# Kernel optimization log

Hardware: AMD Instinct MI355X
Metric: run time of the kernel (lower is better)

Reference implementation:

```python
import math
import jax, jax.numpy as jnp
import numpy as np

MUL = 8      # multiplicity of 0e and 1o in irreps_in/out
KS = 5       # kernel spatial extent (diameter 5, steps 1 -> coords -2..2)
NB = 5       # num_radial_basis
RAD = 2.5    # diameter / 2


def _sus(t):
    # e3nn sus(x) = exp(-1/x) for x>0 else 0
    return jnp.where(t > 0.0, jnp.exp(-1.0 / jnp.where(t > 0.0, t, 1.0)), 0.0)


def _emb_sh():
    c = jnp.arange(-2.0, 3.0)
    lat = jnp.stack(jnp.meshgrid(c, c, c, indexing='ij'), axis=-1)  # (5,5,5,3)
    d = jnp.linalg.norm(lat, axis=-1)
    # soft_one_hot_linspace(basis='smooth_finite', cutoff=True)
    values = jnp.linspace(0.0, RAD, NB + 2)
    step = values[1] - values[0]
    diff = (d[..., None] - values[1:-1]) / step
    emb = 1.14136 * math.exp(2.0) * _sus(diff + 1.0) * _sus(1.0 - diff)  # (5,5,5,NB)
    # real spherical harmonics, lmax=2, normalize=True, normalization='component'
    safe = jnp.where(d > 0.0, d, 1.0)[..., None]
    u = jnp.where(d[..., None] > 0.0, lat / safe, 0.0)
    x, y, z = u[..., 0], u[..., 1], u[..., 2]
    s3, s5, s15 = math.sqrt(3.0), math.sqrt(5.0), math.sqrt(15.0)
    sh = jnp.stack([
        jnp.ones_like(x),
        s3 * x, s3 * y, s3 * z,
        s15 * x * z, s15 * x * y,
        s5 * (y * y - 0.5 * (x * x + z * z)),
        s15 * y * z, (s15 / 2.0) * (z * z - x * x),
    ], axis=-1)  # (5,5,5,9)
    return emb, sh


def _c121():
    # Clebsch-Gordan (w3j) for 1o x 2e -> 1o in the real e3nn basis, built from the
    # orthonormal symmetric-traceless matrix basis matching the l=2 SH component order.
    s2, s6 = math.sqrt(2.0), math.sqrt(6.0)
    S = np.zeros((5, 3, 3))
    S[0, 0, 2] = S[0, 2, 0] = 1.0 / s2            # xz
    S[1, 0, 1] = S[1, 1, 0] = 1.0 / s2            # xy
    S[2] = np.diag([-1.0, 2.0, -1.0]) / s6        # 2y^2 - x^2 - z^2
    S[3, 1, 2] = S[3, 2, 1] = 1.0 / s2            # yz
    S[4] = np.diag([-1.0, 0.0, 1.0]) / s2         # z^2 - x^2
    # w3j(1,2,1)[m,j,k] = S[j,m,k]/sqrt(5)  (fully symmetric since l1+l2+l3 even)
    return jnp.asarray(np.transpose(S, (1, 0, 2)) / math.sqrt(5.0), dtype=jnp.float32)


def _build_kernel(weight, emb, sh, c121, dtype):
    g = (KS, KS, KS)
    W = (emb @ weight) / float(KS * KS * KS)  # (5,5,5,320)
    w1, w2, w3, w4, w5 = [W[..., 64 * i:64 * (i + 1)].reshape(g + (MUL, MUL)) for i in range(5)]
    sh0, sh1, sh2 = sh[..., 0], sh[..., 1:4], sh[..., 4:9]
    pw0 = math.sqrt(1.0 / 16.0)   # output 0e: alpha=1, fan_in=8+8
    pw1 = math.sqrt(3.0 / 24.0)   # output 1o: alpha=3, fan_in=8+8+8
    inv_s3 = 1.0 / math.sqrt(3.0)
    K00 = pw0 * sh0[..., None, None] * w1                                   # (g,u,w)
    K01 = (pw1 * inv_s3) * jnp.einsum('xyzuw,xyzk->xyzuwk', w2, sh1)        # (g,u,w,k)
    K10 = (pw0 * inv_s3) * jnp.einsum('xyzuw,xyzm->xyzumw', w4, sh1)        # (g,u,m,w)
    T = jnp.einsum('xyzj,mjk->xyzmk', sh2, c121)                            # (g,m,k)
    eye3 = jnp.eye(3, dtype=dtype)
    K11 = pw1 * (inv_s3 * jnp.einsum('xyzuw,mk->xyzumwk', sh0[..., None, None] * w3, eye3)
                 + jnp.einsum('xyzuw,xyzmk->xyzumwk', w5, T))               # (g,u,m,w,k)
    D = 4 * MUL
    kern = jnp.zeros(g + (D, D), dtype=dtype)
    kern = kern.at[..., :MUL, :MUL].set(K00)
    kern = kern.at[..., :MUL, MUL:].set(K01.reshape(g + (MUL, 3 * MUL)))
    kern = kern.at[..., MUL:, :MUL].set(K10.reshape(g + (3 * MUL, MUL)))
    kern = kern.at[..., MUL:, MUL:].set(K11.reshape(g + (3 * MUL, 3 * MUL)))
    return jnp.transpose(kern, (4, 3, 0, 1, 2))  # 'xyzio->oixyz'


def reference(x, weight, w_sc0, w_sc1):
    emb, sh = _emb_sh()
    c121 = _c121()
    kern = _build_kernel(weight, emb, sh, c121, x.dtype)
    B, _, X, Y, Z = x.shape
    inv_s8 = 1.0 / math.sqrt(MUL)
    # self-connection: e3nn Linear, 0e->0e and 1o->1o blocks
    x0 = x[:, :MUL]
    x1 = x[:, MUL:].reshape(B, MUL, 3, X, Y, Z)
    sc0 = inv_s8 * jnp.einsum('uv,buxyz->bvxyz', w_sc0, x0)
    sc1 = inv_s8 * jnp.einsum('uv,bumxyz->bvmxyz', w_sc1, x1).reshape(B, 3 * MUL, X, Y, Z)
    sc = jnp.concatenate([sc0, sc1], axis=1)
    conv = jax.lax.conv_general_dilated(
        x, kern, window_strides=(1, 1, 1), padding=[(2, 2)] * 3,
        dimension_numbers=('NCDHW', 'OIDHW', 'NCDHW'))
    return sc + conv


def setup_inputs() -> dict:
    key = jax.random.key(0)
    k1, k2, k3, k4 = jax.random.split(key, 4)
    return {
        'x': jax.random.normal(k1, (2, 32, 64, 64, 64), dtype=jnp.float32),
        'weight': jax.random.normal(k2, (NB, 5 * MUL * MUL), dtype=jnp.float32),
        'w_sc0': jax.random.normal(k3, (MUL, MUL), dtype=jnp.float32),
        'w_sc1': jax.random.normal(k4, (MUL, MUL), dtype=jnp.float32),
    }
```

## Files before the change

kernel.cpp:

```cpp
#include <hip/hip_runtime.h>
#include <math.h>

typedef __attribute__((ext_vector_type(8))) short short8;
typedef __attribute__((ext_vector_type(4))) float f32x4;
typedef __attribute__((ext_vector_type(16))) float f32x16;

#define NTAP 125
#define DCH 32

static __device__ __forceinline__ unsigned short f2bf(float f) {
    union { float f; unsigned u; } v; v.f = f;
    unsigned u = v.u;
    return (unsigned short)((u + 0x7FFFu + ((u >> 16) & 1u)) >> 16);
}

static __device__ __forceinline__ void gld_lds16(const void* g, void* l) {
    __builtin_amdgcn_global_load_lds(
        (const __attribute__((address_space(1))) unsigned int*)g,
        (__attribute__((address_space(3))) unsigned int*)l, 16, 0, 0);
}

__global__ __launch_bounds__(128) void build_kern(
    const float* __restrict__ weight,
    const float* __restrict__ w_sc0,
    const float* __restrict__ w_sc1,
    float* __restrict__ kw)
{
    const int t = blockIdx.x;
    const int dx = t / 25, dy = (t / 5) % 5, dz = t % 5;
    const float px = dx - 2.0f, py = dy - 2.0f, pz = dz - 2.0f;
    const float d = sqrtf(px * px + py * py + pz * pz);

    const float stepv = 2.5f / 6.0f;
    const float embc = 1.14136f * expf(2.0f);
    float emb[5];
#pragma unroll
    for (int n = 0; n < 5; ++n) {
        float diff = (d - stepv * (float)(n + 1)) / stepv;
        float a = diff + 1.0f, bb = 1.0f - diff;
        float v = 0.0f;
        if (a > 0.0f && bb > 0.0f)
            v = embc * expf(-1.0f / a) * expf(-1.0f / bb);
        emb[n] = v;
    }

    const float inv_d = (d > 0.0f) ? 1.0f / d : 0.0f;
    const float ux = px * inv_d, uy = py * inv_d, uz = pz * inv_d;
    const float s3 = 1.73205081f, s5 = 2.23606798f, s15 = 3.87298335f;
    float sh[9];
    sh[0] = 1.0f;
    sh[1] = s3 * ux; sh[2] = s3 * uy; sh[3] = s3 * uz;
    sh[4] = s15 * ux * uz;
    sh[5] = s15 * ux * uy;
    sh[6] = s5 * (uy * uy - 0.5f * (ux * ux + uz * uz));
    sh[7] = s15 * uy * uz;
    sh[8] = 0.5f * s15 * (uz * uz - ux * ux);

    const float i_s2 = 0.70710678f, i_s6 = 0.40824829f, i_s5 = 0.44721360f;
    float T[3][3];
    T[0][0] = i_s5 * (-sh[6] * i_s6 - sh[8] * i_s2);
    T[0][1] = i_s5 * (sh[5] * i_s2);
    T[0][2] = i_s5 * (sh[4] * i_s2);
    T[1][0] = T[0][1];
    T[1][1] = i_s5 * (2.0f * sh[6] * i_s6);
    T[1][2] = i_s5 * (sh[7] * i_s2);
    T[2][0] = T[0][2];
    T[2][1] = T[1][2];
    T[2][2] = i_s5 * (-sh[6] * i_s6 + sh[8] * i_s2);

    __shared__ float Wt[320];
    for (int col = threadIdx.x; col < 320; col += 128) {
        float a = 0.0f;
#pragma unroll
        for (int n = 0; n < 5; ++n) a += emb[n] * weight[n * 320 + col];
        Wt[col] = a * (1.0f / 125.0f);
    }
    __syncthreads();

    const float pw0 = 0.25f;
    const float pw1 = 0.35355339f;
    const float inv_s3 = 0.57735027f;
    const float inv_s8 = 0.35355339f;

    for (int idx = threadIdx.x; idx < 1024; idx += 128) {
        const int o = idx >> 5, i = idx & 31;
        float val;
        if (o < 8) {
            if (i < 8) {
                val = pw0 * Wt[i * 8 + o];
            } else {
                const int u = (i - 8) / 3, m = (i - 8) % 3;
                val = pw0 * inv_s3 * Wt[192 + u * 8 + o] * sh[1 + m];
            }
        } else {
            const int v = (o - 8) / 3, k = (o - 8) % 3;
            if (i < 8) {
                val = pw1 * inv_s3 * Wt[64 + i * 8 + v] * sh[1 + k];
            } else {
                const int u = (i - 8) / 3, m = (i - 8) % 3;
                float tv = Wt[256 + u * 8 + v] * T[m][k];
                if (m == k) tv += inv_s3 * Wt[128 + u * 8 + v];
                val = pw1 * tv;
            }
        }
        if (t == 62) {
            if (o < 8 && i < 8) {
                val += inv_s8 * w_sc0[i * 8 + o];
            } else if (o >= 8 && i >= 8) {
                const int u = (i - 8) / 3, m = (i - 8) % 3;
                const int v = (o - 8) / 3, k = (o - 8) % 3;
                if (m == k) val += inv_s8 * w_sc1[u * 8 + v];
            }
        }
        kw[(i * NTAP + t) * DCH + o] = val;
    }
}

__global__ __launch_bounds__(128) void pack_b(
    const float* __restrict__ kw, unsigned short* __restrict__ kwb)
{
    const int t = blockIdx.x;
    const int tid = threadIdx.x;
    const int kh = tid >> 6, l = tid & 63;
    const int co = l & 31;
    const int cib = kh * 16 + (l >> 5) * 8;
    unsigned short v[8];
#pragma unroll
    for (int j = 0; j < 8; ++j)
        v[j] = f2bf(kw[((cib + j) * NTAP + t) * DCH + co]);
    uint4 o;
    o.x = (unsigned)v[0] | ((unsigned)v[1] << 16);
    o.y = (unsigned)v[2] | ((unsigned)v[3] << 16);
    o.z = (unsigned)v[4] | ((unsigned)v[5] << 16);
    o.w = (unsigned)v[6] | ((unsigned)v[7] << 16);
    *reinterpret_cast<uint4*>(kwb + ((size_t)(t * 2 + kh) * 64 + l) * 8) = o;
}

__global__ __launch_bounds__(256) void xpose(
    const float* __restrict__ x, unsigned short* __restrict__ xt)
{
    const int xx = blockIdx.x, yy = blockIdx.y, b = blockIdx.z;
    const int t = threadIdx.x;
    const int z = t & 63, part = t >> 6;
    const float* src = x + ((((size_t)b * 32) * 64 + xx) * 64 + yy) * 64 + z;
    unsigned short v[8];
#pragma unroll
    for (int j = 0; j < 8; ++j)
        v[j] = f2bf(src[(size_t)(part * 8 + j) * 262144]);
    uint4 o;
    o.x = (unsigned)v[0] | ((unsigned)v[1] << 16);
    o.y = (unsigned)v[2] | ((unsigned)v[3] << 16);
    o.z = (unsigned)v[4] | ((unsigned)v[5] << 16);
    o.w = (unsigned)v[6] | ((unsigned)v[7] << 16);
    *reinterpret_cast<uint4*>(
        xt + ((((size_t)b * 64 + xx) * 64 + yy) * 64 + z) * 32 + part * 8) = o;
}

__global__ void zero_fill(float4* p) {
    p[threadIdx.x] = make_float4(0.f, 0.f, 0.f, 0.f);
}

__global__ __launch_bounds__(512, 2) void conv_mfma(
    const unsigned short* __restrict__ xt,
    const unsigned short* __restrict__ kwb,
    const unsigned short* __restrict__ zpage,
    float* __restrict__ out)
{
    extern __shared__ unsigned short smem[];
    char* lds = (char*)smem;

    const int tid = threadIdx.x;
    const int lane = tid & 63;
    const int wv = tid >> 6;
    const int oyp = wv >> 1, zh = wv & 1;
    const int x0 = blockIdx.x * 4, y0 = blockIdx.y * 8;
    const int b = blockIdx.z;
    const int l31 = lane & 31, hi = lane >> 5;

    int abase[5][2];
#pragma unroll
    for (int dz = 0; dz < 5; ++dz) {
        const int s = zh * 32 + l31 + dz;
#pragma unroll
        for (int kh = 0; kh < 2; ++kh) {
            const int cph = (kh * 2 + hi) ^ ((s >> 1) & 3);
            abase[dz][kh] =
                51200 + ((((oyp * 2 * 68 + s) << 2) | cph) << 4);
        }
    }
    const int bbase = lane * 16;

    int srow[5]; int soff[5]; bool szok[5];
#pragma unroll
    for (int p = 0; p < 5; ++p) {
        const int c = tid + p * 512;
        const int row = c / 272;
        const int rem = c - row * 272;
        const int slot = rem >> 2;
        const int clog = (rem & 3) ^ ((slot >> 1) & 3);
        const int z = slot - 2;
        srow[p] = row;
        szok[p] = ((unsigned)z < 64u);
        soff[p] = row * 2048 + z * 32 + clog * 8;
    }

    int bsrc[7];
#pragma unroll
    for (int k = 0; k < 7; ++k) {
        const int c = tid + k * 512;
        const int tp = c >> 7, rem = c & 127;
        const int dxx = tp / 5, dzz = tp - dxx * 5;
        bsrc[k] = (dxx * 25 + dzz) * 128 + rem;
    }

    auto issue_bs = [&](int dy) {
#pragma unroll
        for (int k = 0; k < 7; ++k) {
            const int c0 = wv * 64 + k * 512;
            if (c0 < 3200) {
                gld_lds16(kwb + ((size_t)(bsrc[k] + dy * 640)) * 8,
                          lds + c0 * 16);
            }
        }
    };

    auto issue_slab = [&](int dyn, int xln, int bufi) {
        const int yyb = y0 + dyn - 2;
        const int xx = x0 + xln - 2;
        const bool xok = ((unsigned)xx < 64u);
        const long long xyb =
            (long long)(b * 64 + xx) * 131072 + (long long)yyb * 2048;
        char* dst = lds + 51200 + bufi * 34816;
#pragma unroll
        for (int p = 0; p < 4; ++p) {
            const int yy = yyb + srow[p];
            const bool ok = xok && ((unsigned)yy < 64u) && szok[p];
            const unsigned short* src = ok ? (xt + xyb + soff[p]) : zpage;
            gld_lds16(src, dst + (wv * 64 + p * 512) * 16);
        }
        if (wv < 2) {
            const int yy = yyb + srow[4];
            const bool ok = xok && ((unsigned)yy < 64u) && szok[4];
            const unsigned short* src = ok ? (xt + xyb + soff[4]) : zpage;
            gld_lds16(src, dst + (wv * 64 + 2048) * 16);
        }
    };

    f32x16 acc[2][4];
#pragma unroll
    for (int oyi = 0; oyi < 2; ++oyi)
#pragma unroll
        for (int ox = 0; ox < 4; ++ox)
#pragma unroll
            for (int e = 0; e < 16; ++e) acc[oyi][ox][e] = 0.0f;

    issue_bs(0);
    issue_slab(0, 0, 0);
    __syncthreads();

    for (int dy = 0; dy < 5; ++dy) {
#pragma unroll
        for (int xl = 0; xl < 8; ++xl) {
            if (xl == 0) {
                if (dy > 0) {
                    issue_bs(dy);
                    __builtin_amdgcn_sched_barrier(0);
                    issue_slab(dy, 1, 1);
                    __builtin_amdgcn_sched_barrier(0);
                    if (wv < 2)
                        asm volatile("s_waitcnt vmcnt(5)" ::: "memory");
                    else
                        asm volatile("s_waitcnt vmcnt(4)" ::: "memory");
                    __builtin_amdgcn_s_barrier();
                    __builtin_amdgcn_sched_barrier(0);
                } else {
                    issue_slab(0, 1, 1);
                }
            } else if (!(dy == 4 && xl == 7)) {
                issue_slab(xl == 7 ? dy + 1 : dy, xl == 7 ? 0 : xl + 1,
                           (xl & 1) ^ 1);
            }

            const int boff = (xl & 1) * 34816;
#pragma unroll
            for (int dz = 0; dz < 5; ++dz) {
#pragma unroll
                for (int kh = 0; kh < 2; ++kh) {
                    const short8 a0 = *reinterpret_cast<const short8*>(
                        lds + abase[dz][kh] + boff);
                    const short8 a1 = *reinterpret_cast<const short8*>(
                        lds + abase[dz][kh] + boff + 4352);
#pragma unroll
                    for (int ox = 0; ox < 4; ++ox) {
                        const int dxv = xl - ox;
                        if (dxv < 0 || dxv > 4) continue;
                        const short8 bf = *reinterpret_cast<const short8*>(
                            lds + bbase + (((dxv * 5 + dz) * 2 + kh) << 10));
                        acc[0][ox] = __builtin_amdgcn_mfma_f32_32x32x16_bf16(
                            a0, bf, acc[0][ox], 0, 0, 0);
                        acc[1][ox] = __builtin_amdgcn_mfma_f32_32x32x16_bf16(
                            a1, bf, acc[1][ox], 0, 0, 0);
                    }
                }
            }
            __syncthreads();
        }
    }

#pragma unroll
    for (int oyi = 0; oyi < 2; ++oyi) {
        const int yy = y0 + oyp * 2 + oyi;
#pragma unroll
        for (int ox = 0; ox < 4; ++ox) {
            float* base = out +
                ((((size_t)b * 32 + l31) * 64 + (x0 + ox)) * 64 + yy) * 64 +
                zh * 32 + hi * 4;
#pragma unroll
            for (int rq = 0; rq < 4; ++rq) {
                f32x4 v = { acc[oyi][ox][rq * 4 + 0], acc[oyi][ox][rq * 4 + 1],
                            acc[oyi][ox][rq * 4 + 2], acc[oyi][ox][rq * 4 + 3] };
                *reinterpret_cast<f32x4*>(base + rq * 8) = v;
            }
        }
    }
}

extern "C" void kernel_launch(void* const* d_in, const int* in_sizes, int n_in,
                              void* d_out, int out_size, void* d_ws, size_t ws_size,
                              hipStream_t stream) {
    const float* x      = (const float*)d_in[0];
    const float* weight = (const float*)d_in[1];
    const float* w_sc0  = (const float*)d_in[2];
    const float* w_sc1  = (const float*)d_in[3];
    float* out = (float*)d_out;

    char* ws = (char*)d_ws;
    unsigned short* xt  = (unsigned short*)ws;
    float*          kwp = (float*)(ws + 33554432);
    unsigned short* kwb = (unsigned short*)(ws + 34066432);
    unsigned short* zpg = (unsigned short*)(ws + 34322432);

    (void)hipFuncSetAttribute((const void*)conv_mfma,
                              hipFuncAttributeMaxDynamicSharedMemorySize,
                              120832);

    hipLaunchKernelGGL(build_kern, dim3(NTAP), dim3(128), 0, stream,
                       weight, w_sc0, w_sc1, kwp);
    hipLaunchKernelGGL(pack_b, dim3(NTAP), dim3(128), 0, stream, kwp, kwb);
    hipLaunchKernelGGL(xpose, dim3(64, 64, 2), dim3(256), 0, stream, x, xt);
    hipLaunchKernelGGL(zero_fill, dim3(1), dim3(256), 0, stream, (float4*)zpg);
    hipLaunchKernelGGL(conv_mfma, dim3(16, 8, 2), dim3(512), 120832, stream,
                       xt, kwb, zpg, out);
}
```

Measured before the change: 147.4 us.

## Triple-buffer input slabs in conv and fuse weight build with bf16 packing

The conv kernel moves from double to triple buffering of the x-slab in LDS (dynamic shared memory grows to 155648 bytes). Loads are issued two steps ahead, and the full __syncthreads after each step becomes a partial vmcnt wait plus s_barrier, so more global-to-LDS latency overlaps with MFMA work. Separately, the kernel build and the bf16 pack are fused into one launch that stages through shared memory, removing a kernel launch and an fp32 workspace round trip. The larger LDS footprint still fits one 512-thread block per CU, and the hand-written waitcnt sequencing must stay correct.

New measurement: 148.8 us. About the same (+0.9%).

```diff
diff --git a/kernel.cpp b/kernel.cpp
--- a/kernel.cpp
+++ b/kernel.cpp
@@ -20,11 +20,11 @@
         (__attribute__((address_space(3))) unsigned int*)l, 16, 0, 0);
 }
 
-__global__ __launch_bounds__(128) void build_kern(
+__global__ __launch_bounds__(128) void build_pack(
     const float* __restrict__ weight,
     const float* __restrict__ w_sc0,
     const float* __restrict__ w_sc1,
-    float* __restrict__ kw)
+    unsigned short* __restrict__ kwb)
 {
     const int t = blockIdx.x;
     const int dx = t / 25, dy = (t / 5) % 5, dz = t % 5;
@@ -69,6 +69,7 @@
     T[2][2] = i_s5 * (-sh[6] * i_s6 + sh[8] * i_s2);
 
     __shared__ float Wt[320];
+    __shared__ float kws[1024];
     for (int col = threadIdx.x; col < 320; col += 128) {
         float a = 0.0f;
 #pragma unroll
@@ -112,14 +113,10 @@
                 if (m == k) val += inv_s8 * w_sc1[u * 8 + v];
             }
         }
-        kw[(i * NTAP + t) * DCH + o] = val;
-    }
-}
-
-__global__ __launch_bounds__(128) void pack_b(
-    const float* __restrict__ kw, unsigned short* __restrict__ kwb)
-{
-    const int t = blockIdx.x;
+        kws[i * 32 + o] = val;
+    }
+    __syncthreads();
+
     const int tid = threadIdx.x;
     const int kh = tid >> 6, l = tid & 63;
     const int co = l & 31;
@@ -127,7 +124,7 @@
     unsigned short v[8];
 #pragma unroll
     for (int j = 0; j < 8; ++j)
-        v[j] = f2bf(kw[((cib + j) * NTAP + t) * DCH + co]);
+        v[j] = f2bf(kws[(cib + j) * 32 + co]);
     uint4 o;
     o.x = (unsigned)v[0] | ((unsigned)v[1] << 16);
     o.y = (unsigned)v[2] | ((unsigned)v[3] << 16);
@@ -224,13 +221,13 @@
         }
     };
 
-    auto issue_slab = [&](int dyn, int xln, int bufi) {
+    auto issue_slab = [&](int dyn, int xln, int dstoff) {
         const int yyb = y0 + dyn - 2;
         const int xx = x0 + xln - 2;
         const bool xok = ((unsigned)xx < 64u);
         const long long xyb =
             (long long)(b * 64 + xx) * 131072 + (long long)yyb * 2048;
-        char* dst = lds + 51200 + bufi * 34816;
+        char* dst = lds + 51200 + dstoff;
 #pragma unroll
         for (int p = 0; p < 4; ++p) {
             const int yy = yyb + srow[p];
@@ -246,6 +243,11 @@
         }
     };
 
+    auto wait_keep_slab = [&]() {
+        if (wv < 2) asm volatile("s_waitcnt vmcnt(5)" ::: "memory");
+        else        asm volatile("s_waitcnt vmcnt(4)" ::: "memory");
+    };
+
     f32x16 acc[2][4];
 #pragma unroll
     for (int oyi = 0; oyi < 2; ++oyi)
@@ -255,41 +257,45 @@
             for (int e = 0; e < 16; ++e) acc[oyi][ox][e] = 0.0f;
 
     issue_bs(0);
+    __builtin_amdgcn_sched_barrier(0);
     issue_slab(0, 0, 0);
-    __syncthreads();
+    __builtin_amdgcn_sched_barrier(0);
+    issue_slab(0, 1, 34816);
+    __builtin_amdgcn_sched_barrier(0);
+    wait_keep_slab();
+    __builtin_amdgcn_s_barrier();
+
+    int rd = 0;
+    int prev = 69632;
 
     for (int dy = 0; dy < 5; ++dy) {
 #pragma unroll
         for (int xl = 0; xl < 8; ++xl) {
-            if (xl == 0) {
-                if (dy > 0) {
-                    issue_bs(dy);
-                    __builtin_amdgcn_sched_barrier(0);
-                    issue_slab(dy, 1, 1);
-                    __builtin_amdgcn_sched_barrier(0);
-                    if (wv < 2)
-                        asm volatile("s_waitcnt vmcnt(5)" ::: "memory");
-                    else
-                        asm volatile("s_waitcnt vmcnt(4)" ::: "memory");
-                    __builtin_amdgcn_s_barrier();
-                    __builtin_amdgcn_sched_barrier(0);
-                } else {
-                    issue_slab(0, 1, 1);
-                }
-            } else if (!(dy == 4 && xl == 7)) {
-                issue_slab(xl == 7 ? dy + 1 : dy, xl == 7 ? 0 : xl + 1,
-                           (xl & 1) ^ 1);
-            }
-
-            const int boff = (xl & 1) * 34816;
+            const bool bdry = (xl == 0) && (dy > 0);
+            if (bdry) {
+                issue_bs(dy);
+                __builtin_amdgcn_sched_barrier(0);
+            }
+            if (!(dy == 4 && xl >= 6)) {
+                const int ndy = (xl >= 6) ? dy + 1 : dy;
+                const int nxl = (xl >= 6) ? xl - 6 : xl + 2;
+                issue_slab(ndy, nxl, prev);
+                __builtin_amdgcn_sched_barrier(0);
+            }
+            if (bdry) {
+                wait_keep_slab();
+                __builtin_amdgcn_s_barrier();
+            }
+
 #pragma unroll
             for (int dz = 0; dz < 5; ++dz) {
 #pragma unroll
                 for (int kh = 0; kh < 2; ++kh) {
-                    const short8 a0 = *reinterpret_cast<const short8*>(
-                        lds + abase[dz][kh] + boff);
-                    const short8 a1 = *reinterpret_cast<const short8*>(
-                        lds + abase[dz][kh] + boff + 4352);
+                    const char* ap = lds + abase[dz][kh] + rd;
+                    const short8 a0 =
+                        *reinterpret_cast<const short8*>(ap);
+                    const short8 a1 =
+                        *reinterpret_cast<const short8*>(ap + 4352);
 #pragma unroll
                     for (int ox = 0; ox < 4; ++ox) {
                         const int dxv = xl - ox;
@@ -303,7 +309,18 @@
                     }
                 }
             }
-            __syncthreads();
+
+            if (dy == 4 && xl >= 6) {
+                asm volatile("s_waitcnt vmcnt(0)" ::: "memory");
+            } else {
+                wait_keep_slab();
+            }
+            if (!(dy == 4 && xl == 7))
+                __builtin_amdgcn_s_barrier();
+
+            const int tmp = rd;
+            rd = (rd == 69632) ? 0 : rd + 34816;
+            prev = tmp;
         }
     }
 
@@ -336,19 +353,17 @@
 
     char* ws = (char*)d_ws;
     unsigned short* xt  = (unsigned short*)ws;
-    float*          kwp = (float*)(ws + 33554432);
-    unsigned short* kwb = (unsigned short*)(ws + 34066432);
-    unsigned short* zpg = (unsigned short*)(ws + 34322432);
+    unsigned short* kwb = (unsigned short*)(ws + 33554432);
+    unsigned short* zpg = (unsigned short*)(ws + 33810432);
 
     (void)hipFuncSetAttribute((const void*)conv_mfma,
                               hipFuncAttributeMaxDynamicSharedMemorySize,
-                              120832);
-
-    hipLaunchKernelGGL(build_kern, dim3(NTAP), dim3(128), 0, stream,
-                       weight, w_sc0, w_sc1, kwp);
-    hipLaunchKernelGGL(pack_b, dim3(NTAP), dim3(128), 0, stream, kwp, kwb);
+                              155648);
+
+    hipLaunchKernelGGL(build_pack, dim3(NTAP), dim3(128), 0, stream,
+                       weight, w_sc0, w_sc1, kwb);
     hipLaunchKernelGGL(xpose, dim3(64, 64, 2), dim3(256), 0, stream, x, xt);
     hipLaunchKernelGGL(zero_fill, dim3(1), dim3(256), 0, stream, (float4*)zpg);
-    hipLaunchKernelGGL(conv_mfma, dim3(16, 8, 2), dim3(512), 120832, stream,
+    hipLaunchKernelGGL(conv_mfma, dim3(16, 8, 2), dim3(512), 155648, stream,
                        xt, kwb, zpg, out);
 }
```
